# Kernel optimization log

Hardware: AMD Instinct MI355X
Metric: run time of the kernel (lower is better)

The kernel has to match this reference:

```python
import jax, jax.numpy as jnp
import numpy as np

N_EMBD = 512
BLOCK = 512
HEADS = 16
HEAD_DIM = N_EMBD // HEADS
EPS = 1e-5


def _layernorm(x, g, b):
    mu = jnp.mean(x, axis=-1, keepdims=True)
    var = jnp.mean(jnp.square(x - mu), axis=-1, keepdims=True)
    return (x - mu) * jax.lax.rsqrt(var + EPS) * g + b


def setup_inputs() -> dict:
    key = jax.random.key(0)
    ks = jax.random.split(key, 12)
    B, T, C, H, D = 64, BLOCK, N_EMBD, HEADS, HEAD_DIM
    s = lambda fan_in: 1.0 / np.sqrt(fan_in)
    return {
        "x": jax.random.normal(ks[0], (B, T, C), dtype=jnp.float32),
        # per-head projections, stored (H, C, D) so y = einsum('btc,hcd->bhtd')
        "Wq": jax.random.normal(ks[1], (H, C, D), dtype=jnp.float32) * s(C),
        "Wk": jax.random.normal(ks[2], (H, C, D), dtype=jnp.float32) * s(C),
        "Wv": jax.random.normal(ks[3], (H, C, D), dtype=jnp.float32) * s(C),
        "Wp": jax.random.normal(ks[4], (C, C), dtype=jnp.float32) * s(C),
        "bp": jnp.zeros((C,), dtype=jnp.float32),
        "W1": jax.random.normal(ks[5], (C, 4 * C), dtype=jnp.float32) * s(C),
        "b1": jnp.zeros((4 * C,), dtype=jnp.float32),
        "W2": jax.random.normal(ks[6], (4 * C, C), dtype=jnp.float32) * s(4 * C),
        "b2": jnp.zeros((C,), dtype=jnp.float32),
        "g_ln1": jnp.ones((C,), dtype=jnp.float32),
        "b_ln1": jnp.zeros((C,), dtype=jnp.float32),
        "g_ln2": jnp.ones((C,), dtype=jnp.float32),
        "b_ln2": jnp.zeros((C,), dtype=jnp.float32),
    }


def reference(x, Wq, Wk, Wv, Wp, bp, W1, b1, W2, b2, g_ln1, b_ln1, g_ln2, b_ln2):
    B, T, C = x.shape
    h = _layernorm(x, g_ln1, b_ln1)
    q = jnp.einsum('btc,hcd->bhtd', h, Wq)
    k = jnp.einsum('btc,hcd->bhtd', h, Wk)
    v = jnp.einsum('btc,hcd->bhtd', h, Wv)
    wei = jnp.einsum('bhtd,bhsd->bhts', q, k) * (HEAD_DIM ** -0.5)
    causal = jnp.tril(jnp.ones((T, T), dtype=bool))
    wei = jnp.where(causal, wei, -jnp.inf)
    wei = jax.nn.softmax(wei, axis=-1)  # dropout = identity (eval mode)
    out = jnp.einsum('bhts,bhsd->bhtd', wei, v)
    out = out.transpose(0, 2, 1, 3).reshape(B, T, C)  # concat heads
    sa = out @ Wp + bp
    x = x + sa
    h2 = _layernorm(x, g_ln2, b_ln2)
    ff = jax.nn.relu(h2 @ W1 + b1) @ W2 + b2
    return x + ff
```

## Files before the change

### kernel.cpp

```cpp
#include <hip/hip_runtime.h>
#include <stdint.h>


typedef __attribute__((ext_vector_type(8))) short bf16x8;
typedef __attribute__((ext_vector_type(4))) short bf16x4;
typedef __attribute__((ext_vector_type(4))) float f32x4;

__device__ __forceinline__ unsigned short f2bf(float x) {
  union { float f; unsigned u; } v; v.f = x;
  unsigned r = v.u + 0x7fff + ((v.u >> 16) & 1);
  return (unsigned short)(r >> 16);
}

#if __has_builtin(__builtin_amdgcn_exp2f)
__device__ __forceinline__ float exp2fast(float x) { return __builtin_amdgcn_exp2f(x); }
#else
__device__ __forceinline__ float exp2fast(float x) { return exp2f(x); }
#endif

__device__ __forceinline__ unsigned cvtpk(float lo, float hi) {
  unsigned r; asm("v_cvt_pk_bf16_f32 %0, %1, %2" : "=v"(r) : "v"(lo), "v"(hi)); return r;
}

__device__ __forceinline__ f32x4 MFMA32(bf16x8 a, bf16x8 b, f32x4 c) {
  return __builtin_amdgcn_mfma_f32_16x16x32_bf16(a, b, c, 0, 0, 0);
}

#if __has_builtin(__builtin_amdgcn_mfma_f32_16x16x16bf16_1k)
__device__ __forceinline__ f32x4 MFMA16(bf16x4 a, bf16x4 b, f32x4 c) {
  return __builtin_amdgcn_mfma_f32_16x16x16bf16_1k(a, b, c, 0, 0, 0);
}
#else
__device__ __forceinline__ f32x4 MFMA16(bf16x4 a, bf16x4 b, f32x4 c) {
  f32x4 d;
  asm volatile("v_mfma_f32_16x16x16_bf16 %0, %1, %2, %3\n\ts_nop 7\n\ts_nop 3"
               : "=v"(d) : "v"(a), "v"(b), "v"(c));
  return d;
}
#endif

__device__ __forceinline__ void gload_lds16(const void* g, void* l) {
  __builtin_amdgcn_global_load_lds(
      (const __attribute__((address_space(1))) unsigned int*)(uintptr_t)g,
      (__attribute__((address_space(3))) unsigned int*)(unsigned)(uintptr_t)l,
      16, 0, 0);
}

#define WAITV0() do { asm volatile("s_waitcnt vmcnt(0)" ::: "memory"); } while (0)
#define SBAR()   __builtin_amdgcn_s_barrier()
#define SCHED0() __builtin_amdgcn_sched_barrier(0)

__global__ __launch_bounds__(256) void prep_qkv_w(
    const float* __restrict__ Wq, const float* __restrict__ Wk,
    const float* __restrict__ Wv, unsigned short* __restrict__ dst)
{
  __shared__ float tile[64 * 33];
  const int b = blockIdx.x;
  const int q = b / 128, hh = (b >> 3) & 15, kt = (b & 7) << 6;
  const float* W = (q == 0) ? Wq : ((q == 1) ? Wk : Wv);
  const int t = threadIdx.x;
  const int rr = t >> 2, ch = (t & 3) << 3;
  const float* sp = W + ((size_t)hh * 512 + kt + rr) * 32 + ch;
  float4 v0 = *(const float4*)(sp), v1 = *(const float4*)(sp + 4);
  float* dp = &tile[rr * 33 + ch];
  dp[0] = v0.x; dp[1] = v0.y; dp[2] = v0.z; dp[3] = v0.w;
  dp[4] = v1.x; dp[5] = v1.y; dp[6] = v1.z; dp[7] = v1.w;
  __syncthreads();
  const int d = t >> 3, toct = (t & 7) << 3;
  bf16x8 o;
#pragma unroll
  for (int j = 0; j < 8; ++j) o[j] = (short)f2bf(tile[(toct + j) * 33 + d]);
  *(bf16x8*)(dst + ((size_t)q * 512 + hh * 32 + d) * 512 + kt + toct) = o;
}

__global__ __launch_bounds__(256) void transpose_cast(
    const float* __restrict__ src, unsigned short* __restrict__ dst, int Kd, int Nd)
{
  __shared__ float tile[64 * 65];
  const int nk = Kd >> 6;
  const int kt = (blockIdx.x % nk) << 6, nt = (blockIdx.x / nk) << 6;
  const int t = threadIdx.x;
  const int rr = t >> 2, ch = (t & 3) << 4;
  const float* sp = src + (size_t)(kt + rr) * Nd + nt + ch;
  float* dp = &tile[rr * 65 + ch];
#pragma unroll
  for (int c = 0; c < 4; ++c) {
    float4 v = *(const float4*)(sp + c * 4);
    dp[c * 4 + 0] = v.x; dp[c * 4 + 1] = v.y; dp[c * 4 + 2] = v.z; dp[c * 4 + 3] = v.w;
  }
  __syncthreads();
  const int nn = t >> 2, c2 = (t & 3) << 4;
  bf16x8 o0, o1;
#pragma unroll
  for (int j = 0; j < 8; ++j) {
    o0[j] = (short)f2bf(tile[(c2 + j) * 65 + nn]);
    o1[j] = (short)f2bf(tile[(c2 + 8 + j) * 65 + nn]);
  }
  unsigned short* op = dst + (size_t)(nt + nn) * Kd + kt + c2;
  *(bf16x8*)(op) = o0;
  *(bf16x8*)(op + 8) = o1;
}

__global__ __launch_bounds__(256) void ln_kernel(
    const float* __restrict__ x, const float* __restrict__ g,
    const float* __restrict__ b, unsigned short* __restrict__ out)
{
  const int lane = threadIdx.x & 63;
  const size_t row = (size_t)blockIdx.x * 4 + (threadIdx.x >> 6);
  const float* xp = x + row * 512 + lane * 8;
  float xv[8] __attribute__((aligned(16)));
  *(float4*)(xv)     = *(const float4*)(xp);
  *(float4*)(xv + 4) = *(const float4*)(xp + 4);
  float s = 0.f, s2 = 0.f;
#pragma unroll
  for (int j = 0; j < 8; ++j) { s += xv[j]; s2 += xv[j] * xv[j]; }
#pragma unroll
  for (int m = 1; m < 64; m <<= 1) { s += __shfl_xor(s, m); s2 += __shfl_xor(s2, m); }
  float mean = s * (1.f / 512.f);
  float rstd = rsqrtf(fmaxf(s2 * (1.f / 512.f) - mean * mean, 0.f) + 1e-5f);
  float gv[8] __attribute__((aligned(16))), bv[8] __attribute__((aligned(16)));
  *(float4*)(gv)     = *(const float4*)(g + lane * 8);
  *(float4*)(gv + 4) = *(const float4*)(g + lane * 8 + 4);
  *(float4*)(bv)     = *(const float4*)(b + lane * 8);
  *(float4*)(bv + 4) = *(const float4*)(b + lane * 8 + 4);
  bf16x8 o;
#pragma unroll
  for (int j = 0; j < 8; ++j) o[j] = (short)f2bf((xv[j] - mean) * rstd * gv[j] + bv[j]);
  *(bf16x8*)(out + row * 512 + lane * 8) = o;
}

__global__ __launch_bounds__(256) void vt_kernel(
    const unsigned short* __restrict__ vnat, unsigned short* __restrict__ vt)
{
  __shared__ unsigned short tile[64 * 36];
  const int bh = blockIdx.x >> 3, tt = (blockIdx.x & 7) << 6;
  const int tid = threadIdx.x;
  const int rr = tid >> 2, ch = tid & 3;
  bf16x8 v = *(const bf16x8*)(vnat + ((size_t)bh * 512 + tt + rr) * 32 + ch * 8);
  unsigned short* dst = &tile[rr * 36 + ch * 8];
#pragma unroll
  for (int j = 0; j < 8; ++j) dst[j] = (unsigned short)v[j];
  __syncthreads();
  const int d = tid >> 3, toct = (tid & 7) << 3;
  union { unsigned short s[8]; bf16x8 v8; } o;
#pragma unroll
  for (int j = 0; j < 8; ++j) o.s[j] = tile[(toct + j) * 36 + d];
  *(bf16x8*)(vt + ((size_t)bh * 32 + d) * 512 + tt + toct) = o.v8;
}

template <int MODE, int P, int KT, int NBY>
__device__ __forceinline__ void gemm_persist(
    const unsigned short* __restrict__ A, const unsigned short* __restrict__ Bt,
    int N,
    unsigned short* __restrict__ obf, float* __restrict__ of32,
    const float* __restrict__ bias, const float* __restrict__ resid,
    unsigned short* __restrict__ vout)
{
  constexpr int K = KT * 64;
  constexpr int TOT = P * KT;
  __shared__ __align__(16) unsigned short As[2][256 * 64];
  __shared__ __align__(16) unsigned short Bs[2][256 * 64];
  const int tid = threadIdx.x, lane = tid & 63, wid = tid >> 6;
  const int wr = wid >> 2, wc = wid & 3;
  const int r = lane & 15, hq = lane >> 4;

  const int tau0 = (blockIdx.x & 7) * (32 * P) + (blockIdx.x >> 3) * P;

  const int srow = wid * 32 + (lane >> 3);
  const int schunk = ((lane & 7) ^ ((lane >> 3) & 7)) * 8;

  auto STAGE_A = [&](int g2) {
    const int m2 = g2 / KT, kt2 = g2 % KT;
    const int bx = (tau0 + m2) / NBY;
    const unsigned short* src = A + (size_t)(bx * 256 + srow) * K + kt2 * 64 + schunk;
    char* dst = (char*)(&As[g2 & 1][0]) + wid * 4096;
#pragma unroll
    for (int g = 0; g < 4; ++g) gload_lds16(src + (size_t)g * 8 * K, dst + g * 1024);
  };
  auto STAGE_B = [&](int g2) {
    const int m2 = g2 / KT, kt2 = g2 % KT;
    const int tau = tau0 + m2;
    const int by = tau - (tau / NBY) * NBY;
    const unsigned short* src = Bt + (size_t)(by * 256 + srow) * K + kt2 * 64 + schunk;
    char* dst = (char*)(&Bs[g2 & 1][0]) + wid * 4096;
#pragma unroll
    for (int g = 0; g < 4; ++g) gload_lds16(src + (size_t)g * 8 * K, dst + g * 1024);
  };

  const int x0 = ((hq) ^ (r & 7)) * 16;
  const int x1 = ((4 + hq) ^ (r & 7)) * 16;
  const int abase = (wr * 128 + r) * 128;
  const int bbase = (wc * 64 + r) * 128;

  f32x4 acc[8][4] = {};

  STAGE_A(0); STAGE_B(0);
  WAITV0(); SCHED0();
  SBAR();

#pragma unroll 1
  for (int p = 0; p < P; ++p) {
#pragma unroll 2
    for (int t = 0; t < KT; ++t) {
      const int g = p * KT + t;
      if (g + 1 < TOT) { STAGE_A(g + 1); STAGE_B(g + 1); }
      const char* Ab = (const char*)(&As[g & 1][0]);
      const char* Bb = (const char*)(&Bs[g & 1][0]);
      bf16x8 bf[4][2];
#pragma unroll
      for (int n = 0; n < 4; ++n) {
        bf[n][0] = *(const bf16x8*)(Bb + bbase + n * 2048 + x0);
        bf[n][1] = *(const bf16x8*)(Bb + bbase + n * 2048 + x1);
      }
#pragma unroll
      for (int m = 0; m < 8; ++m) {
        const bf16x8 a0 = *(const bf16x8*)(Ab + abase + m * 2048 + x0);
        const bf16x8 a1 = *(const bf16x8*)(Ab + abase + m * 2048 + x1);
#pragma unroll
        for (int n = 0; n < 4; ++n) {
          acc[m][n] = MFMA32(a0, bf[n][0], acc[m][n]);
          acc[m][n] = MFMA32(a1, bf[n][1], acc[m][n]);
        }
      }
      WAITV0(); SCHED0();
      SBAR();
    }

    {
      const int tau = tau0 + p;
      const int bx = tau / NBY, by = tau - bx * NBY;
      const int brow = bx << 8, bcol = by << 8;
#pragma unroll
      for (int m = 0; m < 8; ++m)
#pragma unroll
        for (int n = 0; n < 4; ++n) {
          const int row0 = brow + wr * 128 + m * 16 + hq * 4;
          const int col = bcol + wc * 64 + n * 16 + r;
#pragma unroll
          for (int q2 = 0; q2 < 4; ++q2) {
            const int row = row0 + q2;
            float v = acc[m][n][q2];
            if (MODE == 1) {
              const int which = col >> 9, hh = (col >> 5) & 15, dd = col & 31;
              const int bb = row >> 9, tt = row & 511;
              const size_t off = ((((size_t)bb) * 16 + hh) * 512 + tt) * 32 + dd;
              if (which < 2) {
                if (which == 0) v *= 0.25503521f;
                obf[(size_t)which * 16777216 + off] = f2bf(v);
              } else
                vout[off] = f2bf(v);
            } else if (MODE == 2) {
              v += bias[col] + resid[(size_t)row * N + col];
              of32[(size_t)row * N + col] = v;
            } else if (MODE == 3) {
              v = fmaxf(v + bias[col], 0.f);
              obf[(size_t)row * N + col] = f2bf(v);
            }
            acc[m][n][q2] = 0.f;
          }
        }
    }
  }
}

__global__ __launch_bounds__(512, 2) void qkv_gemm(
    const unsigned short* __restrict__ A, const unsigned short* __restrict__ Bt,
    unsigned short* __restrict__ obf, unsigned short* __restrict__ vout)
{ gemm_persist<1, 3, 8, 6>(A, Bt, 1536, obf, nullptr, nullptr, nullptr, vout); }

__global__ __launch_bounds__(512, 2) void proj_gemm(
    const unsigned short* __restrict__ A, const unsigned short* __restrict__ Bt,
    float* __restrict__ of32, const float* __restrict__ bias,
    const float* __restrict__ resid)
{ gemm_persist<2, 1, 8, 2>(A, Bt, 512, nullptr, of32, bias, resid, nullptr); }

__global__ __launch_bounds__(512, 2) void ffn1_gemm(
    const unsigned short* __restrict__ A, const unsigned short* __restrict__ Bt,
    unsigned short* __restrict__ obf, const float* __restrict__ bias)
{ gemm_persist<3, 4, 8, 8>(A, Bt, 2048, obf, nullptr, bias, nullptr, nullptr); }

__global__ __launch_bounds__(512, 2) void ffn2_gemm(
    const unsigned short* __restrict__ A, const unsigned short* __restrict__ Bt,
    float* __restrict__ of32, const float* __restrict__ bias,
    const float* __restrict__ resid)
{ gemm_persist<2, 1, 32, 2>(A, Bt, 512, nullptr, of32, bias, resid, nullptr); }

__global__ __launch_bounds__(512, 4) void attn_kernel(
    const unsigned short* __restrict__ Qb, const unsigned short* __restrict__ Kb,
    const unsigned short* __restrict__ Vt, unsigned short* __restrict__ att)
{
  __shared__ __align__(16) unsigned short Ks[512 * 32];
  __shared__ __align__(16) unsigned short Vs[32 * 512];
  const int tid = threadIdx.x, lane = tid & 63, wid = tid >> 6;
  const int bh = blockIdx.x;
  const int r = lane & 15, hq = lane >> 4;
  const unsigned short* Kg = Kb + (size_t)bh * (512 * 32);
  const unsigned short* Vg = Vt + (size_t)bh * (32 * 512);
#pragma unroll
  for (int it = 0; it < 4; ++it) {
    const int c = it * 512 + tid;
    gload_lds16(Kg + c * 8, (char*)Ks + (it * 512 + wid * 64) * 16);
    const int d = c >> 6, sb = c & 63;
    gload_lds16(Vg + d * 512 + (sb ^ (d & 15)) * 8, (char*)Vs + (it * 512 + wid * 64) * 16);
  }
  __syncthreads();

  const f32x4 z = {0.f, 0.f, 0.f, 0.f};
  for (int p = 0; p < 4; ++p) {
    const int t0 = (((p >> 1) << 4) + ((p & 1) ? 15 - wid : wid)) << 4;
    const bf16x8 qf = *(const bf16x8*)(Qb + ((size_t)bh * 512 + t0 + r) * 32 + hq * 8);
    f32x4 o0 = z, o1 = z;
    float m = -1e30f, l = 0.f;
    const int s0m = t0 & ~31;
    for (int s0 = 0; s0 <= s0m; s0 += 32) {
      f32x4 st0 = MFMA32(*(const bf16x8*)((const char*)Ks + (s0 + r) * 64 + hq * 16), qf, z);
      f32x4 st1 = MFMA32(*(const bf16x8*)((const char*)Ks + (s0 + 16 + r) * 64 + hq * 16), qf, z);
      if (s0 == s0m) {
        const int qq = t0 + r;
#pragma unroll
        for (int j = 0; j < 4; ++j) {
          if (s0 + 4 * hq + j > qq)      st0[j] = -1e30f;
          if (s0 + 16 + 4 * hq + j > qq) st1[j] = -1e30f;
        }
      }
      float mx = fmaxf(fmaxf(fmaxf(st0[0], st0[1]), fmaxf(st0[2], st0[3])),
                       fmaxf(fmaxf(st1[0], st1[1]), fmaxf(st1[2], st1[3])));
      mx = fmaxf(mx, __shfl_xor(mx, 16));
      mx = fmaxf(mx, __shfl_xor(mx, 32));
      if (!__all(mx <= m + 8.f)) {
        const float mn = fmaxf(m, mx);
        const float f = exp2fast(m - mn);
        m = mn; l *= f; o0 *= f; o1 *= f;
      }
      float p0[4], p1[4];
#pragma unroll
      for (int j = 0; j < 4; ++j) {
        p0[j] = exp2fast(st0[j] - m);
        p1[j] = exp2fast(st1[j] - m);
      }
      float rs = ((p0[0] + p0[1]) + (p0[2] + p0[3])) + ((p1[0] + p1[1]) + (p1[2] + p1[3]));
      rs += __shfl_xor(rs, 16);
      rs += __shfl_xor(rs, 32);
      l += rs;
      union { unsigned u[2]; bf16x4 v; } a0, a1;
      a0.u[0] = cvtpk(p0[0], p0[1]); a0.u[1] = cvtpk(p0[2], p0[3]);
      a1.u[0] = cvtpk(p1[0], p1[1]); a1.u[1] = cvtpk(p1[2], p1[3]);
      const int lb = (s0 >> 3) + (hq >> 1);
      const char* vb = (const char*)Vs + (hq & 1) * 8;
      o0 = MFMA16(a0.v, *(const bf16x4*)(vb + r * 1024 + ((lb) ^ r) * 16), o0);
      o0 = MFMA16(a1.v, *(const bf16x4*)(vb + r * 1024 + ((lb + 2) ^ r) * 16), o0);
      o1 = MFMA16(a0.v, *(const bf16x4*)(vb + (r + 16) * 1024 + ((lb) ^ r) * 16), o1);
      o1 = MFMA16(a1.v, *(const bf16x4*)(vb + (r + 16) * 1024 + ((lb + 2) ^ r) * 16), o1);
    }
    const size_t ob = ((size_t)(bh >> 4) * 512) * 512 + (size_t)((bh & 15) * 32);
#pragma unroll
    for (int j = 0; j < 4; ++j) {
      const float li = 1.f / __shfl(l, 4 * hq + j);
      const size_t rowb = ob + (size_t)(t0 + 4 * hq + j) * 512;
      att[rowb + r]      = f2bf(o0[j] * li);
      att[rowb + 16 + r] = f2bf(o1[j] * li);
    }
  }
}

extern "C" void kernel_launch(void* const* d_in, const int* in_sizes, int n_in,
                              void* d_out, int out_size, void* d_ws, size_t ws_size,
                              hipStream_t stream)
{
  const float* x   = (const float*)d_in[0];
  const float* Wq  = (const float*)d_in[1];
  const float* Wk  = (const float*)d_in[2];
  const float* Wv  = (const float*)d_in[3];
  const float* Wp  = (const float*)d_in[4];
  const float* bp  = (const float*)d_in[5];
  const float* W1  = (const float*)d_in[6];
  const float* b1  = (const float*)d_in[7];
  const float* W2  = (const float*)d_in[8];
  const float* b2  = (const float*)d_in[9];
  const float* g1  = (const float*)d_in[10];
  const float* bb1 = (const float*)d_in[11];
  const float* g2  = (const float*)d_in[12];
  const float* bb2 = (const float*)d_in[13];
  float* out = (float*)d_out;

  char* ws = (char*)d_ws;
  unsigned short* h    = (unsigned short*)(ws);
  unsigned short* wqkv = (unsigned short*)(ws + 33554432);
  unsigned short* wp   = (unsigned short*)(ws + 35127296);
  unsigned short* w1   = (unsigned short*)(ws + 35651584);
  unsigned short* w2   = (unsigned short*)(ws + 37748736);
  unsigned short* qk   = (unsigned short*)(ws + 39845888);
  unsigned short* vt   = qk + (size_t)2 * 16777216;
  unsigned short* att  = vt + 16777216;
  unsigned short* vnat = att;
  unsigned short* mid  = qk;
  if (ws_size < 174063616) return;

  prep_qkv_w<<<384, 256, 0, stream>>>(Wq, Wk, Wv, wqkv);
  transpose_cast<<<64, 256, 0, stream>>>(Wp, wp, 512, 512);
  transpose_cast<<<256, 256, 0, stream>>>(W1, w1, 512, 2048);
  transpose_cast<<<256, 256, 0, stream>>>(W2, w2, 2048, 512);

  ln_kernel<<<8192, 256, 0, stream>>>(x, g1, bb1, h);

  qkv_gemm<<<256, 512, 0, stream>>>(h, wqkv, qk, vnat);

  vt_kernel<<<8192, 256, 0, stream>>>(vnat, vt);

  attn_kernel<<<1024, 512, 0, stream>>>(qk, qk + 16777216, vt, att);

  proj_gemm<<<256, 512, 0, stream>>>(att, wp, out, bp, x);

  ln_kernel<<<8192, 256, 0, stream>>>(out, g2, bb2, h);

  ffn1_gemm<<<256, 512, 0, stream>>>(h, w1, mid, b1);

  ffn2_gemm<<<256, 512, 0, stream>>>(mid, w2, out, b2, out);
}
```

Baseline: 408.5 us.

## Replace persistent 256x256 double-buffered GEMM with non-persistent 128x128 tiles

Swaps the persistent, double-buffered 256x256-tile GEMM (512 threads, several tiles per block) for a simple 128x128-tile kernel with 256 threads, one tile per block and many more blocks. Loads are single-buffered with two __syncthreads per K step, and K and the grid shape become runtime parameters. The aim is higher occupancy and better load balance across CUs. In exchange it gives up global-to-LDS prefetch overlap and halves data reuse per tile, which raises global and L2 traffic.

```diff
diff --git a/kernel.cpp b/kernel.cpp
--- a/kernel.cpp
+++ b/kernel.cpp
@@ -45,10 +45,6 @@
       (__attribute__((address_space(3))) unsigned int*)(unsigned)(uintptr_t)l,
       16, 0, 0);
 }
-
-#define WAITV0() do { asm volatile("s_waitcnt vmcnt(0)" ::: "memory"); } while (0)
-#define SBAR()   __builtin_amdgcn_s_barrier()
-#define SCHED0() __builtin_amdgcn_sched_barrier(0)
 
 __global__ __launch_bounds__(256) void prep_qkv_w(
     const float* __restrict__ Wq, const float* __restrict__ Wk,
@@ -148,142 +144,123 @@
   *(bf16x8*)(vt + ((size_t)bh * 32 + d) * 512 + tt + toct) = o.v8;
 }
 
-template <int MODE, int P, int KT, int NBY>
-__device__ __forceinline__ void gemm_persist(
-    const unsigned short* __restrict__ A, const unsigned short* __restrict__ Bt,
-    int N,
+template <int MODE>
+__device__ __forceinline__ void gemm128_body(
+    const unsigned short* __restrict__ A, const unsigned short* __restrict__ Bt,
+    int N, int K, int nby,
     unsigned short* __restrict__ obf, float* __restrict__ of32,
     const float* __restrict__ bias, const float* __restrict__ resid,
     unsigned short* __restrict__ vout)
 {
-  constexpr int K = KT * 64;
-  constexpr int TOT = P * KT;
-  __shared__ __align__(16) unsigned short As[2][256 * 64];
-  __shared__ __align__(16) unsigned short Bs[2][256 * 64];
+  __shared__ __align__(16) unsigned short As[128 * 64];
+  __shared__ __align__(16) unsigned short Bs[128 * 64];
   const int tid = threadIdx.x, lane = tid & 63, wid = tid >> 6;
-  const int wr = wid >> 2, wc = wid & 3;
+  const int wr = wid >> 1, wc = wid & 1;
   const int r = lane & 15, hq = lane >> 4;
 
-  const int tau0 = (blockIdx.x & 7) * (32 * P) + (blockIdx.x >> 3) * P;
-
-  const int srow = wid * 32 + (lane >> 3);
+  const int qq = gridDim.x >> 3;
+  const int swz = (blockIdx.x & 7) * qq + (blockIdx.x >> 3);
+  const int bx = swz / nby, by = swz - bx * nby;
+  const int brow = bx << 7, bcol = by << 7;
+  const int nkt = K >> 6;
+
+  const int srow = wid * 8 + (lane >> 3);
   const int schunk = ((lane & 7) ^ ((lane >> 3) & 7)) * 8;
-
-  auto STAGE_A = [&](int g2) {
-    const int m2 = g2 / KT, kt2 = g2 % KT;
-    const int bx = (tau0 + m2) / NBY;
-    const unsigned short* src = A + (size_t)(bx * 256 + srow) * K + kt2 * 64 + schunk;
-    char* dst = (char*)(&As[g2 & 1][0]) + wid * 4096;
-#pragma unroll
-    for (int g = 0; g < 4; ++g) gload_lds16(src + (size_t)g * 8 * K, dst + g * 1024);
-  };
-  auto STAGE_B = [&](int g2) {
-    const int m2 = g2 / KT, kt2 = g2 % KT;
-    const int tau = tau0 + m2;
-    const int by = tau - (tau / NBY) * NBY;
-    const unsigned short* src = Bt + (size_t)(by * 256 + srow) * K + kt2 * 64 + schunk;
-    char* dst = (char*)(&Bs[g2 & 1][0]) + wid * 4096;
-#pragma unroll
-    for (int g = 0; g < 4; ++g) gload_lds16(src + (size_t)g * 8 * K, dst + g * 1024);
-  };
-
-  const int x0 = ((hq) ^ (r & 7)) * 16;
+  const unsigned short* Abase = A + (size_t)(brow + srow) * K + schunk;
+  const unsigned short* Bbase = Bt + (size_t)(bcol + srow) * K + schunk;
+
+  const int x0 = (hq ^ (r & 7)) * 16;
   const int x1 = ((4 + hq) ^ (r & 7)) * 16;
-  const int abase = (wr * 128 + r) * 128;
+  const int abase = (wr * 64 + r) * 128;
   const int bbase = (wc * 64 + r) * 128;
 
-  f32x4 acc[8][4] = {};
-
-  STAGE_A(0); STAGE_B(0);
-  WAITV0(); SCHED0();
-  SBAR();
-
-#pragma unroll 1
-  for (int p = 0; p < P; ++p) {
-#pragma unroll 2
-    for (int t = 0; t < KT; ++t) {
-      const int g = p * KT + t;
-      if (g + 1 < TOT) { STAGE_A(g + 1); STAGE_B(g + 1); }
-      const char* Ab = (const char*)(&As[g & 1][0]);
-      const char* Bb = (const char*)(&Bs[g & 1][0]);
-      bf16x8 bf[4][2];
+  f32x4 acc[4][4] = {};
+
+  for (int t = 0; t < nkt; ++t) {
+    {
+      const unsigned short* as_ = Abase + t * 64;
+      const unsigned short* bs_ = Bbase + t * 64;
+      char* al_ = (char*)As + wid * 1024;
+      char* bl_ = (char*)Bs + wid * 1024;
+#pragma unroll
+      for (int g = 0; g < 4; ++g) {
+        gload_lds16(as_ + (size_t)g * 32 * K, al_ + g * 4096);
+        gload_lds16(bs_ + (size_t)g * 32 * K, bl_ + g * 4096);
+      }
+    }
+    __syncthreads();
+    bf16x8 bf[4][2];
+#pragma unroll
+    for (int n = 0; n < 4; ++n) {
+      bf[n][0] = *(const bf16x8*)((const char*)Bs + bbase + n * 2048 + x0);
+      bf[n][1] = *(const bf16x8*)((const char*)Bs + bbase + n * 2048 + x1);
+    }
+#pragma unroll
+    for (int m = 0; m < 4; ++m) {
+      const bf16x8 a0 = *(const bf16x8*)((const char*)As + abase + m * 2048 + x0);
+      const bf16x8 a1 = *(const bf16x8*)((const char*)As + abase + m * 2048 + x1);
 #pragma unroll
       for (int n = 0; n < 4; ++n) {
-        bf[n][0] = *(const bf16x8*)(Bb + bbase + n * 2048 + x0);
-        bf[n][1] = *(const bf16x8*)(Bb + bbase + n * 2048 + x1);
-      }
-#pragma unroll
-      for (int m = 0; m < 8; ++m) {
-        const bf16x8 a0 = *(const bf16x8*)(Ab + abase + m * 2048 + x0);
-        const bf16x8 a1 = *(const bf16x8*)(Ab + abase + m * 2048 + x1);
-#pragma unroll
-        for (int n = 0; n < 4; ++n) {
-          acc[m][n] = MFMA32(a0, bf[n][0], acc[m][n]);
-          acc[m][n] = MFMA32(a1, bf[n][1], acc[m][n]);
+        acc[m][n] = MFMA32(a0, bf[n][0], acc[m][n]);
+        acc[m][n] = MFMA32(a1, bf[n][1], acc[m][n]);
+      }
+    }
+    __syncthreads();
+  }
+
+#pragma unroll
+  for (int m = 0; m < 4; ++m)
+#pragma unroll
+    for (int n = 0; n < 4; ++n) {
+      const int row0 = brow + wr * 64 + m * 16 + hq * 4;
+      const int col = bcol + wc * 64 + n * 16 + r;
+#pragma unroll
+      for (int q2 = 0; q2 < 4; ++q2) {
+        const int row = row0 + q2;
+        float v = acc[m][n][q2];
+        if (MODE == 1) {
+          const int which = col >> 9, hh = (col >> 5) & 15, dd = col & 31;
+          const int bb = row >> 9, tt = row & 511;
+          const size_t off = ((((size_t)bb) * 16 + hh) * 512 + tt) * 32 + dd;
+          if (which < 2) {
+            if (which == 0) v *= 0.25503521f;
+            obf[(size_t)which * 16777216 + off] = f2bf(v);
+          } else
+            vout[off] = f2bf(v);
+        } else if (MODE == 2) {
+          v += bias[col] + resid[(size_t)row * N + col];
+          of32[(size_t)row * N + col] = v;
+        } else if (MODE == 3) {
+          v = fmaxf(v + bias[col], 0.f);
+          obf[(size_t)row * N + col] = f2bf(v);
         }
       }
-      WAITV0(); SCHED0();
-      SBAR();
-    }
-
-    {
-      const int tau = tau0 + p;
-      const int bx = tau / NBY, by = tau - bx * NBY;
-      const int brow = bx << 8, bcol = by << 8;
-#pragma unroll
-      for (int m = 0; m < 8; ++m)
-#pragma unroll
-        for (int n = 0; n < 4; ++n) {
-          const int row0 = brow + wr * 128 + m * 16 + hq * 4;
-          const int col = bcol + wc * 64 + n * 16 + r;
-#pragma unroll
-          for (int q2 = 0; q2 < 4; ++q2) {
-            const int row = row0 + q2;
-            float v = acc[m][n][q2];
-            if (MODE == 1) {
-              const int which = col >> 9, hh = (col >> 5) & 15, dd = col & 31;
-              const int bb = row >> 9, tt = row & 511;
-              const size_t off = ((((size_t)bb) * 16 + hh) * 512 + tt) * 32 + dd;
-              if (which < 2) {
-                if (which == 0) v *= 0.25503521f;
-                obf[(size_t)which * 16777216 + off] = f2bf(v);
-              } else
-                vout[off] = f2bf(v);
-            } else if (MODE == 2) {
-              v += bias[col] + resid[(size_t)row * N + col];
-              of32[(size_t)row * N + col] = v;
-            } else if (MODE == 3) {
-              v = fmaxf(v + bias[col], 0.f);
-              obf[(size_t)row * N + col] = f2bf(v);
-            }
-            acc[m][n][q2] = 0.f;
-          }
-        }
-    }
-  }
-}
-
-__global__ __launch_bounds__(512, 2) void qkv_gemm(
-    const unsigned short* __restrict__ A, const unsigned short* __restrict__ Bt,
-    unsigned short* __restrict__ obf, unsigned short* __restrict__ vout)
-{ gemm_persist<1, 3, 8, 6>(A, Bt, 1536, obf, nullptr, nullptr, nullptr, vout); }
-
-__global__ __launch_bounds__(512, 2) void proj_gemm(
-    const unsigned short* __restrict__ A, const unsigned short* __restrict__ Bt,
-    float* __restrict__ of32, const float* __restrict__ bias,
-    const float* __restrict__ resid)
-{ gemm_persist<2, 1, 8, 2>(A, Bt, 512, nullptr, of32, bias, resid, nullptr); }
-
-__global__ __launch_bounds__(512, 2) void ffn1_gemm(
-    const unsigned short* __restrict__ A, const unsigned short* __restrict__ Bt,
-    unsigned short* __restrict__ obf, const float* __restrict__ bias)
-{ gemm_persist<3, 4, 8, 8>(A, Bt, 2048, obf, nullptr, bias, nullptr, nullptr); }
-
-__global__ __launch_bounds__(512, 2) void ffn2_gemm(
-    const unsigned short* __restrict__ A, const unsigned short* __restrict__ Bt,
-    float* __restrict__ of32, const float* __restrict__ bias,
-    const float* __restrict__ resid)
-{ gemm_persist<2, 1, 32, 2>(A, Bt, 512, nullptr, of32, bias, resid, nullptr); }
+    }
+}
+
+__global__ __launch_bounds__(256, 3) void qkv_gemm(
+    const unsigned short* __restrict__ A, const unsigned short* __restrict__ Bt,
+    int N, int K, int nby, unsigned short* __restrict__ obf,
+    unsigned short* __restrict__ vout)
+{ gemm128_body<1>(A, Bt, N, K, nby, obf, nullptr, nullptr, nullptr, vout); }
+
+__global__ __launch_bounds__(256, 3) void proj_gemm(
+    const unsigned short* __restrict__ A, const unsigned short* __restrict__ Bt,
+    int N, int K, int nby, float* __restrict__ of32,
+    const float* __restrict__ bias, const float* __restrict__ resid)
+{ gemm128_body<2>(A, Bt, N, K, nby, nullptr, of32, bias, resid, nullptr); }
+
+__global__ __launch_bounds__(256, 3) void ffn1_gemm(
+    const unsigned short* __restrict__ A, const unsigned short* __restrict__ Bt,
+    int N, int K, int nby, unsigned short* __restrict__ obf,
+    const float* __restrict__ bias)
+{ gemm128_body<3>(A, Bt, N, K, nby, obf, nullptr, bias, nullptr, nullptr); }
+
+__global__ __launch_bounds__(256, 3) void ffn2_gemm(
+    const unsigned short* __restrict__ A, const unsigned short* __restrict__ Bt,
+    int N, int K, int nby, float* __restrict__ of32,
+    const float* __restrict__ bias, const float* __restrict__ resid)
+{ gemm128_body<2>(A, Bt, N, K, nby, nullptr, of32, bias, resid, nullptr); }
 
 __global__ __launch_bounds__(512, 4) void attn_kernel(
     const unsigned short* __restrict__ Qb, const unsigned short* __restrict__ Kb,
@@ -403,17 +380,17 @@
 
   ln_kernel<<<8192, 256, 0, stream>>>(x, g1, bb1, h);
 
-  qkv_gemm<<<256, 512, 0, stream>>>(h, wqkv, qk, vnat);
+  qkv_gemm<<<3072, 256, 0, stream>>>(h, wqkv, 1536, 512, 12, qk, vnat);
 
   vt_kernel<<<8192, 256, 0, stream>>>(vnat, vt);
 
   attn_kernel<<<1024, 512, 0, stream>>>(qk, qk + 16777216, vt, att);
 
-  proj_gemm<<<256, 512, 0, stream>>>(att, wp, out, bp, x);
+  proj_gemm<<<1024, 256, 0, stream>>>(att, wp, 512, 512, 4, out, bp, x);
 
   ln_kernel<<<8192, 256, 0, stream>>>(out, g2, bb2, h);
 
-  ffn1_gemm<<<256, 512, 0, stream>>>(h, w1, mid, b1);
-
-  ffn2_gemm<<<256, 512, 0, stream>>>(mid, w2, out, b2, out);
-}
+  ffn1_gemm<<<4096, 256, 0, stream>>>(h, w1, 2048, 512, 16, mid, b1);
+
+  ffn2_gemm<<<1024, 256, 0, stream>>>(mid, w2, 512, 2048, 4, out, b2, out);
+}
```

After: 380.3 us. 6.9% less time.
